# Performance work log

Hardware: AMD Instinct MI355X
Metric: run time of the kernel (lower is better)

The kernel has to match this reference:

```python
import jax, jax.numpy as jnp
import numpy as np

B_SIZE, STEPS, UNITS = 128, 1024, 1024
E = 2 * STEPS              # model_internal_dim = expand_factor * model_input_dims
DT_RANK = (STEPS + 1) // 2 # math.ceil(model_input_dims / 2)
N = UNITS // 2             # model_states
COND = 512                 # conditioning feature size
K = 4                      # conv kernel size


def setup_inputs() -> dict:
    key = jax.random.key(0)
    ks = jax.random.split(key, 12)
    s = lambda k, shape, fan: jax.random.normal(k, shape, jnp.float32) / np.sqrt(fan)
    return {
        "x": jax.random.normal(ks[0], (B_SIZE, 1, STEPS), jnp.float32),
        "c": jax.random.normal(ks[1], (B_SIZE, COND), jnp.float32),
        "ln_g": jnp.ones((STEPS,), jnp.float32),
        "ln_b": jnp.zeros((STEPS,), jnp.float32),
        "W_in": s(ks[2], (STEPS, 2 * E), STEPS),
        "conv_w": s(ks[3], (K, 1, E), K),
        "conv_b": jnp.zeros((E,), jnp.float32),
        "W_x": s(ks[4], (E, DT_RANK + 2 * N), E),
        "W_dt": s(ks[5], (DT_RANK, E), DT_RANK),
        "b_dt": jnp.zeros((E,), jnp.float32),
        "A_log": jnp.log(jnp.tile(jnp.arange(1, N + 1, dtype=jnp.float32), (E, 1))),
        "D": jnp.ones((E,), jnp.float32),
        "W_out": s(ks[6], (E, STEPS), E),
        "b_out": jnp.zeros((STEPS,), jnp.float32),
        "W_d": s(ks[7], (STEPS, N), STEPS),
        "b_d": jnp.zeros((N,), jnp.float32),
        "W_f": s(ks[8], (COND, 2 * N), COND),
        "b_f": jnp.zeros((2 * N,), jnp.float32),
        "W_o": s(ks[9], (N, STEPS), N),
        "b_o": jnp.zeros((STEPS,), jnp.float32),
    }


def _selective_scan(u, delta, A, Bm, Cm, D):
    # u, delta: (b,l,e); A: (e,n); Bm, Cm: (b,l,n); D: (e,)
    dA = jnp.exp(jnp.einsum('ble,en->blen', delta, A))        # discretized A
    dBu = jnp.einsum('ble,ble,bln->blen', delta, u, Bm)       # discretized B*u

    def step(h, t):
        dA_t, dBu_t, C_t = t
        h = dA_t * h + dBu_t                                  # (b,e,n)
        return h, jnp.einsum('ben,bn->be', h, C_t)

    h0 = jnp.zeros((dA.shape[0], dA.shape[2], dA.shape[3]), dA.dtype)
    _, ys = jax.lax.scan(step, h0, (dA.transpose(1, 0, 2, 3),
                                    dBu.transpose(1, 0, 2, 3),
                                    Cm.transpose(1, 0, 2)))
    y = ys.transpose(1, 0, 2)                                 # (b,l,e)
    return y + u * D


def reference(x, c, ln_g, ln_b, W_in, conv_w, conv_b, W_x, W_dt, b_dt,
              A_log, D, W_out, b_out, W_d, b_d, W_f, b_f, W_o, b_o):
    # --- ResidualBlock: LayerNorm -> MambaBlock -> + x ---
    mu = jnp.mean(x, -1, keepdims=True)
    var = jnp.var(x, -1, keepdims=True)
    h = (x - mu) * jax.lax.rsqrt(var + 1e-5) * ln_g + ln_b
    xz = h @ W_in                                             # (b,l,2E)
    xi, res = jnp.split(xz, 2, axis=-1)
    xc = jax.lax.conv_general_dilated(
        xi, conv_w, window_strides=(1,), padding=[(K - 1, 0)],
        dimension_numbers=('NWC', 'WIO', 'NWC'), feature_group_count=E) + conv_b
    u = jax.nn.silu(xc)
    x_dbl = u @ W_x                                           # (b,l,dt_rank+2N)
    d_r, Bm, Cm = jnp.split(x_dbl, [DT_RANK, DT_RANK + N], axis=-1)
    delta = jax.nn.softplus(d_r @ W_dt + b_dt)                # (b,l,E)
    A = -jnp.exp(A_log)
    y = _selective_scan(u, delta, A, Bm, Cm, D)
    y = y * jax.nn.silu(res)                                  # gating branch
    mamba_out = y @ W_out + b_out + x                         # residual add
    # --- Dense(model_states, gelu) then squeeze seq dim ---
    z = jax.nn.gelu(mamba_out @ W_d + b_d, approximate=False)
    z = jnp.squeeze(z, axis=1)                                # (b, N)
    # --- FiLM conditioning ---
    gb = c @ W_f + b_f
    g, b = jnp.split(gb, 2, axis=-1)
    z = z * g + b
    # --- output projection back to steps ---
    return z @ W_o + b_o
```

## Files before the change

kernel.cpp:

```cpp
#include <hip/hip_runtime.h>
#include <math.h>

#define E_DIM 2048

typedef __attribute__((ext_vector_type(8))) short short8;
typedef __attribute__((ext_vector_type(4))) float floatx4;

__device__ __forceinline__ float siluf(float v) { return v / (1.f + expf(-v)); }

__device__ __forceinline__ short f2bf(float f) {
    unsigned u = __float_as_uint(f);
    u += 0x7fffu + ((u >> 16) & 1u);
    return (short)(u >> 16);
}

__global__ __launch_bounds__(256) void ln_zero_kernel(const float* __restrict__ x,
                                                      const float* __restrict__ g,
                                                      const float* __restrict__ be,
                                                      const float* __restrict__ c,
                                                      short* __restrict__ h_bf,
                                                      short* __restrict__ c_bf,
                                                      float4* __restrict__ zbase,
                                                      int zTotal) {
    int tid = threadIdx.x;
    if (blockIdx.x < 128) {
        int b = blockIdx.x;
        __shared__ float sdata[256];
        const float* xr = x + b * 1024;
        float v[4];
        float s = 0.f;
#pragma unroll
        for (int i = 0; i < 4; ++i) { v[i] = xr[tid + i * 256]; s += v[i]; }
        sdata[tid] = s; __syncthreads();
        for (int st = 128; st > 0; st >>= 1) { if (tid < st) sdata[tid] += sdata[tid + st]; __syncthreads(); }
        float mu = sdata[0] * (1.f / 1024.f);
        __syncthreads();
        float s2 = 0.f;
#pragma unroll
        for (int i = 0; i < 4; ++i) { float d = v[i] - mu; s2 += d * d; }
        sdata[tid] = s2; __syncthreads();
        for (int st = 128; st > 0; st >>= 1) { if (tid < st) sdata[tid] += sdata[tid + st]; __syncthreads(); }
        float var = sdata[0] * (1.f / 1024.f);
        float inv = rsqrtf(var + 1e-5f);
        short* hr = h_bf + b * 1024;
#pragma unroll
        for (int i = 0; i < 4; ++i) {
            int j = tid + i * 256;
            hr[j] = f2bf((v[i] - mu) * inv * g[j] + be[j]);
        }
        const float* cr = c + b * 512;
        short* cbr = c_bf + b * 512;
        for (int j = tid; j < 512; j += 256) cbr[j] = f2bf(cr[j]);
    } else {
        int base = (blockIdx.x - 128) * 2048 + tid;
        int stride = (gridDim.x - 128) * 2048;
        for (int idx = base; idx < zTotal; idx += stride) {
#pragma unroll
            for (int i = 0; i < 8; ++i) {
                int k = idx + i * 256;
                if (k < zTotal) zbase[k] = (float4){0.f, 0.f, 0.f, 0.f};
            }
        }
    }
}

template<int MODE>
__device__ __forceinline__ short8 load_a_frag(const void* __restrict__ A, int lda, int r, int j0,
                                              const float* __restrict__ aux0,
                                              const float* __restrict__ aux1,
                                              const float* __restrict__ aux2) {
    if constexpr (MODE == 0) {
        return *(const short8*)((const short*)A + (size_t)r * lda + j0);
    } else {
        const float* p = (const float*)A + (size_t)r * lda + j0;
        float v[8];
        if constexpr (MODE == 1) {
#pragma unroll
            for (int i = 0; i < 8; ++i) v[i] = siluf(p[i] * aux0[j0 + i] + aux1[j0 + i]);
        } else if constexpr (MODE == 2) {
#pragma unroll
            for (int i = 0; i < 8; ++i) v[i] = p[i];
        } else if constexpr (MODE == 3) {
#pragma unroll
            for (int i = 0; i < 8; ++i) v[i] = p[i] + aux0[j0 + i] + aux1[(size_t)r * lda + j0 + i];
        } else {
#pragma unroll
            for (int i = 0; i < 8; ++i) {
                float t = p[i] + aux0[j0 + i];
                float zg = 0.5f * t * (1.f + erff(t * 0.70710678118654752f));
                float gq = aux1[(size_t)r * 1024 + j0 + i] + aux2[j0 + i];
                float bb = aux1[(size_t)r * 1024 + 512 + j0 + i] + aux2[512 + j0 + i];
                v[i] = zg * gq + bb;
            }
        }
        short8 s;
#pragma unroll
        for (int i = 0; i < 8; ++i) s[i] = f2bf(v[i]);
        return s;
    }
}

template<int MODE>
__global__ __launch_bounds__(256) void gemm_mfma(const void* __restrict__ A, int lda,
                                                 const float* __restrict__ aux0,
                                                 const float* __restrict__ aux1,
                                                 const float* __restrict__ aux2,
                                                 const float* __restrict__ B, int ldb,
                                                 float* __restrict__ C, int ldc,
                                                 int kChunk) {
    const int tid = threadIdx.x;
    const int w = tid >> 6;
    const int l = tid & 63;
    const int lane15 = l & 15;
    const int lgrp = l >> 4;
    const int n0 = blockIdx.x * 64;
    const int k0 = blockIdx.z * kChunk;

    const int r0 = w * 32 + lane15;
    const float* Bp = B + (size_t)(k0 + lgrp * 8) * ldb + n0 + lane15;

    floatx4 acc[2][4];
#pragma unroll
    for (int i = 0; i < 2; ++i)
#pragma unroll
        for (int j = 0; j < 4; ++j) acc[i][j] = (floatx4)0.f;

    for (int ks = 0; ks < kChunk; ks += 32) {
        int j0 = k0 + ks + lgrp * 8;
        short8 a0 = load_a_frag<MODE>(A, lda, r0, j0, aux0, aux1, aux2);
        short8 a1 = load_a_frag<MODE>(A, lda, r0 + 16, j0, aux0, aux1, aux2);
        float bv[4][8];
#pragma unroll
        for (int i = 0; i < 8; ++i) {
            const float* Br = Bp + i * ldb;
#pragma unroll
            for (int nt = 0; nt < 4; ++nt) bv[nt][i] = Br[nt * 16];
        }
        Bp += 32 * (size_t)ldb;
        short8 vb[4];
#pragma unroll
        for (int nt = 0; nt < 4; ++nt)
#pragma unroll
            for (int i = 0; i < 8; ++i) vb[nt][i] = f2bf(bv[nt][i]);
#pragma unroll
        for (int nt = 0; nt < 4; ++nt) {
            acc[0][nt] = __builtin_amdgcn_mfma_f32_16x16x32_bf16(a0, vb[nt], acc[0][nt], 0, 0, 0);
            acc[1][nt] = __builtin_amdgcn_mfma_f32_16x16x32_bf16(a1, vb[nt], acc[1][nt], 0, 0, 0);
        }
    }
    const int rbase = w * 32 + lgrp * 4;
#pragma unroll
    for (int mf = 0; mf < 2; ++mf)
#pragma unroll
        for (int nt = 0; nt < 4; ++nt)
#pragma unroll
            for (int r = 0; r < 4; ++r)
                atomicAdd(&C[(rbase + mf * 16 + r) * ldc + n0 + nt * 16 + lane15], acc[mf][nt][r]);
}

__global__ __launch_bounds__(256) void e3_kernel(const float* __restrict__ dacc,
                                                 const float* __restrict__ b_dt,
                                                 const float* __restrict__ xz,
                                                 const float* __restrict__ convw3,
                                                 const float* __restrict__ convb,
                                                 const float* __restrict__ xdbl,
                                                 const float* __restrict__ Dv,
                                                 short* __restrict__ y_bf) {
    int b = blockIdx.x;
    int tid = threadIdx.x;
    __shared__ float sdata[256];
    const float* row = xdbl + b * 1536;
    float s = 0.f;
    for (int n = tid; n < 512; n += 256) s += row[512 + n] * row[1024 + n];
    sdata[tid] = s; __syncthreads();
    for (int st = 128; st > 0; st >>= 1) { if (tid < st) sdata[tid] += sdata[tid + st]; __syncthreads(); }
    float svec = sdata[0];
    const float* xzr = xz + b * 4096;
    const float* dar = dacc + b * 2048;
    short* yr = y_bf + b * 2048;
#pragma unroll
    for (int ii = 0; ii < 8; ++ii) {
        int j = tid + ii * 256;
        float t = dar[j] + b_dt[j];
        float delta = fmaxf(t, 0.f) + log1pf(expf(-fabsf(t)));
        float u = siluf(xzr[j] * convw3[j] + convb[j]);
        float sr = siluf(xzr[2048 + j]);
        yr[j] = f2bf(u * (delta * svec + Dv[j]) * sr);
    }
}

__global__ __launch_bounds__(256) void e6_kernel(const float* __restrict__ oa,
                                                 const float* __restrict__ b_o,
                                                 float* __restrict__ out) {
    int idx = blockIdx.x * 256 + threadIdx.x;
    int j = idx & 1023;
    out[idx] = oa[idx] + b_o[j];
}

extern "C" void kernel_launch(void* const* d_in, const int* in_sizes, int n_in,
                              void* d_out, int out_size, void* d_ws, size_t ws_size,
                              hipStream_t stream) {
    (void)in_sizes; (void)n_in; (void)out_size; (void)ws_size;
    const float* x     = (const float*)d_in[0];
    const float* c     = (const float*)d_in[1];
    const float* ln_g  = (const float*)d_in[2];
    const float* ln_b  = (const float*)d_in[3];
    const float* W_in  = (const float*)d_in[4];
    const float* convw = (const float*)d_in[5];
    const float* convb = (const float*)d_in[6];
    const float* W_x   = (const float*)d_in[7];
    const float* W_dt  = (const float*)d_in[8];
    const float* b_dt  = (const float*)d_in[9];
    const float* Dv    = (const float*)d_in[11];
    const float* W_out = (const float*)d_in[12];
    const float* b_out = (const float*)d_in[13];
    const float* W_d   = (const float*)d_in[14];
    const float* b_d   = (const float*)d_in[15];
    const float* W_f   = (const float*)d_in[16];
    const float* b_f   = (const float*)d_in[17];
    const float* W_o   = (const float*)d_in[18];
    const float* b_o   = (const float*)d_in[19];
    float* out = (float*)d_out;

    char* ws = (char*)d_ws;
    size_t off = 0;
    auto allocf = [&](size_t nElem) { float* p = (float*)(ws + off); off += nElem * sizeof(float); return p; };
    auto allocs = [&](size_t nElem) { short* p = (short*)(ws + off); off += nElem * sizeof(short); return p; };
    float* xz_acc   = allocf(128 * 4096);
    float* xdbl_acc = allocf(128 * 1536);
    float* dacc     = allocf(128 * 2048);
    float* mo_acc   = allocf(128 * 1024);
    float* zd_acc   = allocf(128 * 512);
    float* gb_acc   = allocf(128 * 1024);
    float* out_acc  = allocf(128 * 1024);
    size_t accBytes = off;
    int zTotal = (int)(accBytes / 16);
    short* h_bf   = allocs(128 * 1024);
    short* c_bf   = allocs(128 * 512);
    short* y_bf   = allocs(128 * 2048);

    ln_zero_kernel<<<128 + 176, 256, 0, stream>>>(x, ln_g, ln_b, c, h_bf, c_bf,
                                                  (float4*)d_ws, zTotal);
    gemm_mfma<0><<<dim3(64, 1, 4), 256, 0, stream>>>(h_bf, 1024, nullptr, nullptr, nullptr,
                                                     W_in, 4096, xz_acc, 4096, 256);
    gemm_mfma<0><<<dim3(16, 1, 8), 256, 0, stream>>>(c_bf, 512, nullptr, nullptr, nullptr,
                                                     W_f, 1024, gb_acc, 1024, 64);
    gemm_mfma<1><<<dim3(24, 1, 8), 256, 0, stream>>>(xz_acc, 4096, convw + 3 * E_DIM, convb, nullptr,
                                                     W_x, 1536, xdbl_acc, 1536, 256);
    gemm_mfma<2><<<dim3(32, 1, 8), 256, 0, stream>>>(xdbl_acc, 1536, nullptr, nullptr, nullptr,
                                                     W_dt, 2048, dacc, 2048, 64);
    e3_kernel<<<128, 256, 0, stream>>>(dacc, b_dt, xz_acc, convw + 3 * E_DIM, convb,
                                       xdbl_acc, Dv, y_bf);
    gemm_mfma<0><<<dim3(16, 1, 8), 256, 0, stream>>>(y_bf, 2048, nullptr, nullptr, nullptr,
                                                     W_out, 1024, mo_acc, 1024, 256);
    gemm_mfma<3><<<dim3(8, 1, 16), 256, 0, stream>>>(mo_acc, 1024, b_out, x, nullptr,
                                                     W_d, 512, zd_acc, 512, 64);
    gemm_mfma<4><<<dim3(16, 1, 8), 256, 0, stream>>>(zd_acc, 512, b_d, gb_acc, b_f,
                                                     W_o, 1024, out_acc, 1024, 64);
    e6_kernel<<<(128 * 1024) / 256, 256, 0, stream>>>(out_acc, b_o, out);
}
```

Before: 103.9 us.

## Fuse pipeline into one persistent kernel with grid barriers and split-K partial buffers

Replaces the chain of ten kernel launches with a single persistent kernel of 256 blocks. Stages are separated by atomic-counter grid barriers. Split-K results are no longer accumulated with float atomics into zeroed buffers. Each K-slice writes a private partial buffer, and the consumer stage sums the slices, which removes the zeroing pass and atomic contention. The cost is extra partial-buffer memory traffic, barrier spin overhead, and reliance on all 256 blocks being co-resident.

```diff
diff --git a/kernel.cpp b/kernel.cpp
--- a/kernel.cpp
+++ b/kernel.cpp
@@ -1,10 +1,10 @@
 #include <hip/hip_runtime.h>
 #include <math.h>
 
-#define E_DIM 2048
-
 typedef __attribute__((ext_vector_type(8))) short short8;
 typedef __attribute__((ext_vector_type(4))) float floatx4;
+
+#define NBLK 256
 
 __device__ __forceinline__ float siluf(float v) { return v / (1.f + expf(-v)); }
 
@@ -14,18 +14,142 @@
     return (short)(u >> 16);
 }
 
-__global__ __launch_bounds__(256) void ln_zero_kernel(const float* __restrict__ x,
-                                                      const float* __restrict__ g,
-                                                      const float* __restrict__ be,
-                                                      const float* __restrict__ c,
-                                                      short* __restrict__ h_bf,
-                                                      short* __restrict__ c_bf,
-                                                      float4* __restrict__ zbase,
-                                                      int zTotal) {
-    int tid = threadIdx.x;
-    if (blockIdx.x < 128) {
-        int b = blockIdx.x;
-        __shared__ float sdata[256];
+__global__ void init_kernel(int* bar) {
+    if (threadIdx.x < 16) bar[threadIdx.x] = 0;
+}
+
+__device__ __forceinline__ void gbar(int* bar, int i) {
+    __syncthreads();
+    if (threadIdx.x == 0) {
+        __threadfence();
+        int old = __hip_atomic_fetch_add(&bar[i], 1, __ATOMIC_ACQ_REL, __HIP_MEMORY_SCOPE_AGENT);
+        if (old != NBLK - 1) {
+            while (__hip_atomic_load(&bar[i], __ATOMIC_RELAXED, __HIP_MEMORY_SCOPE_AGENT) < NBLK)
+                __builtin_amdgcn_s_sleep(1);
+        }
+        __threadfence();
+    }
+    __syncthreads();
+}
+
+template<int MODE, int NSUM>
+__device__ __forceinline__ short8 a_frag(const void* __restrict__ A, int lda, size_t ss,
+                                         int r, int j0,
+                                         const float* __restrict__ aux0,
+                                         const float* __restrict__ aux1) {
+    if constexpr (MODE == 0) {
+        return *(const short8*)((const short*)A + (size_t)r * lda + j0);
+    } else {
+        const float* Af = (const float*)A;
+        size_t base = (size_t)r * lda + j0;
+        float v[8];
+#pragma unroll
+        for (int i = 0; i < 8; ++i) {
+            float t;
+            if constexpr (MODE == 1) {
+                t = Af[base + i] + Af[ss + base + i];
+                t = siluf(t * aux0[j0 + i] + aux1[j0 + i]);
+            } else {
+                t = 0.f;
+#pragma unroll
+                for (int s = 0; s < NSUM; ++s) t += Af[(size_t)s * ss + base + i];
+                if constexpr (MODE == 3) t += aux0[j0 + i] + aux1[base + i];
+            }
+            v[i] = t;
+        }
+        short8 sv;
+#pragma unroll
+        for (int i = 0; i < 8; ++i) sv[i] = f2bf(v[i]);
+        return sv;
+    }
+}
+
+template<int MODE, int NSUM>
+__device__ __forceinline__ void gemm_stage(const void* __restrict__ A, int lda, size_t ss,
+                                           const float* __restrict__ aux0,
+                                           const float* __restrict__ aux1,
+                                           const float* __restrict__ B, int ldb,
+                                           float* __restrict__ Cs, int ldc,
+                                           int n0, int k0, int kSteps) {
+    const int tid = threadIdx.x;
+    const int w = tid >> 6;
+    const int l = tid & 63;
+    const int lane15 = l & 15;
+    const int lgrp = l >> 4;
+    const int r0 = w * 32 + lane15;
+    const float* Bp = B + (size_t)(k0 + lgrp * 8) * ldb + n0 + lane15;
+
+    floatx4 acc[2][4];
+#pragma unroll
+    for (int i = 0; i < 2; ++i)
+#pragma unroll
+        for (int j = 0; j < 4; ++j) acc[i][j] = (floatx4)0.f;
+
+    for (int s = 0; s < kSteps; ++s) {
+        int j0 = k0 + s * 32 + lgrp * 8;
+        short8 a0 = a_frag<MODE, NSUM>(A, lda, ss, r0, j0, aux0, aux1);
+        short8 a1 = a_frag<MODE, NSUM>(A, lda, ss, r0 + 16, j0, aux0, aux1);
+        float bv[4][8];
+#pragma unroll
+        for (int i = 0; i < 8; ++i) {
+            const float* Br = Bp + (size_t)i * ldb;
+#pragma unroll
+            for (int nt = 0; nt < 4; ++nt) bv[nt][i] = Br[nt * 16];
+        }
+        Bp += 32 * (size_t)ldb;
+        short8 vb[4];
+#pragma unroll
+        for (int nt = 0; nt < 4; ++nt)
+#pragma unroll
+            for (int i = 0; i < 8; ++i) vb[nt][i] = f2bf(bv[nt][i]);
+#pragma unroll
+        for (int nt = 0; nt < 4; ++nt) {
+            acc[0][nt] = __builtin_amdgcn_mfma_f32_16x16x32_bf16(a0, vb[nt], acc[0][nt], 0, 0, 0);
+            acc[1][nt] = __builtin_amdgcn_mfma_f32_16x16x32_bf16(a1, vb[nt], acc[1][nt], 0, 0, 0);
+        }
+    }
+    const int rbase = w * 32 + lgrp * 4;
+#pragma unroll
+    for (int mf = 0; mf < 2; ++mf)
+#pragma unroll
+        for (int nt = 0; nt < 4; ++nt)
+#pragma unroll
+            for (int r = 0; r < 4; ++r)
+                Cs[(size_t)(rbase + mf * 16 + r) * ldc + n0 + nt * 16 + lane15] = acc[mf][nt][r];
+}
+
+__global__ __launch_bounds__(256, 2) void uber_kernel(
+        const float* __restrict__ x, const float* __restrict__ c,
+        const float* __restrict__ ln_g, const float* __restrict__ ln_b,
+        const float* __restrict__ W_in, const float* __restrict__ cw3,
+        const float* __restrict__ cb, const float* __restrict__ W_x,
+        const float* __restrict__ W_dt, const float* __restrict__ b_dt,
+        const float* __restrict__ Dv, const float* __restrict__ W_out,
+        const float* __restrict__ b_out, const float* __restrict__ W_d,
+        const float* __restrict__ b_d, const float* __restrict__ W_f,
+        const float* __restrict__ b_f, const float* __restrict__ W_o,
+        const float* __restrict__ b_o, float* __restrict__ out,
+        int* __restrict__ bar,
+        short* __restrict__ h_bf, short* __restrict__ c_bf,
+        float* __restrict__ xz_p, float* __restrict__ gb_p,
+        float* __restrict__ xdbl_p, float* __restrict__ dacc_p,
+        short* __restrict__ y_bf, float* __restrict__ mo_p,
+        float* __restrict__ zd_p, short* __restrict__ z_bf,
+        float* __restrict__ out_p) {
+    const int bid = blockIdx.x;
+    const int tid = threadIdx.x;
+    __shared__ float sdata[256];
+
+    const size_t XZ_SL = (size_t)128 * 4096;
+    const size_t GB_SL = (size_t)128 * 1024;
+    const size_t XD_SL = (size_t)128 * 1536;
+    const size_t DA_SL = (size_t)128 * 2048;
+    const size_t MO_SL = (size_t)128 * 1024;
+    const size_t ZD_SL = (size_t)128 * 512;
+    const size_t OU_SL = (size_t)128 * 1024;
+
+    if (bid < 128) {
+        int b = bid;
         const float* xr = x + b * 1024;
         float v[4];
         float s = 0.f;
@@ -40,161 +164,129 @@
         for (int i = 0; i < 4; ++i) { float d = v[i] - mu; s2 += d * d; }
         sdata[tid] = s2; __syncthreads();
         for (int st = 128; st > 0; st >>= 1) { if (tid < st) sdata[tid] += sdata[tid + st]; __syncthreads(); }
-        float var = sdata[0] * (1.f / 1024.f);
-        float inv = rsqrtf(var + 1e-5f);
+        float inv = rsqrtf(sdata[0] * (1.f / 1024.f) + 1e-5f);
         short* hr = h_bf + b * 1024;
 #pragma unroll
         for (int i = 0; i < 4; ++i) {
             int j = tid + i * 256;
-            hr[j] = f2bf((v[i] - mu) * inv * g[j] + be[j]);
-        }
+            hr[j] = f2bf((v[i] - mu) * inv * ln_g[j] + ln_b[j]);
+        }
+    } else {
+        int b = bid - 128;
         const float* cr = c + b * 512;
         short* cbr = c_bf + b * 512;
-        for (int j = tid; j < 512; j += 256) cbr[j] = f2bf(cr[j]);
+        cbr[tid] = f2bf(cr[tid]);
+        cbr[tid + 256] = f2bf(cr[tid + 256]);
+    }
+    gbar(bar, 0);
+
+    if (bid < 128) {
+        int nb = bid >> 1, ks = bid & 1;
+        gemm_stage<0, 0>(h_bf, 1024, 0, nullptr, nullptr, W_in, 4096,
+                         xz_p + (size_t)ks * XZ_SL, 4096, nb * 64, ks * 512, 16);
     } else {
-        int base = (blockIdx.x - 128) * 2048 + tid;
-        int stride = (gridDim.x - 128) * 2048;
-        for (int idx = base; idx < zTotal; idx += stride) {
-#pragma unroll
-            for (int i = 0; i < 8; ++i) {
-                int k = idx + i * 256;
-                if (k < zTotal) zbase[k] = (float4){0.f, 0.f, 0.f, 0.f};
+        int t = bid - 128;
+        int nb = t >> 3, ks = t & 7;
+        gemm_stage<0, 0>(c_bf, 512, 0, nullptr, nullptr, W_f, 1024,
+                         gb_p + (size_t)ks * GB_SL, 1024, nb * 64, ks * 64, 2);
+    }
+    gbar(bar, 1);
+
+    if (bid < 192) {
+        int nb = bid >> 3, ks = bid & 7;
+        gemm_stage<1, 2>(xz_p, 4096, XZ_SL, cw3, cb, W_x, 1536,
+                         xdbl_p + (size_t)ks * XD_SL, 1536, nb * 64, ks * 256, 8);
+    }
+    gbar(bar, 2);
+
+    {
+        int nb = bid >> 3, ks = bid & 7;
+        gemm_stage<2, 8>(xdbl_p, 1536, XD_SL, nullptr, nullptr, W_dt, 2048,
+                         dacc_p + (size_t)ks * DA_SL, 2048, nb * 64, ks * 64, 2);
+    }
+    gbar(bar, 3);
+
+    {
+        int row = bid >> 1, half = bid & 1;
+        float s = 0.f;
+#pragma unroll
+        for (int q = 0; q < 2; ++q) {
+            int n = tid + q * 256;
+            float bm = 0.f, cm = 0.f;
+#pragma unroll
+            for (int sl = 0; sl < 8; ++sl) {
+                bm += xdbl_p[(size_t)sl * XD_SL + (size_t)row * 1536 + 512 + n];
+                cm += xdbl_p[(size_t)sl * XD_SL + (size_t)row * 1536 + 1024 + n];
             }
-        }
-    }
-}
-
-template<int MODE>
-__device__ __forceinline__ short8 load_a_frag(const void* __restrict__ A, int lda, int r, int j0,
-                                              const float* __restrict__ aux0,
-                                              const float* __restrict__ aux1,
-                                              const float* __restrict__ aux2) {
-    if constexpr (MODE == 0) {
-        return *(const short8*)((const short*)A + (size_t)r * lda + j0);
-    } else {
-        const float* p = (const float*)A + (size_t)r * lda + j0;
-        float v[8];
-        if constexpr (MODE == 1) {
-#pragma unroll
-            for (int i = 0; i < 8; ++i) v[i] = siluf(p[i] * aux0[j0 + i] + aux1[j0 + i]);
-        } else if constexpr (MODE == 2) {
-#pragma unroll
-            for (int i = 0; i < 8; ++i) v[i] = p[i];
-        } else if constexpr (MODE == 3) {
-#pragma unroll
-            for (int i = 0; i < 8; ++i) v[i] = p[i] + aux0[j0 + i] + aux1[(size_t)r * lda + j0 + i];
-        } else {
-#pragma unroll
-            for (int i = 0; i < 8; ++i) {
-                float t = p[i] + aux0[j0 + i];
-                float zg = 0.5f * t * (1.f + erff(t * 0.70710678118654752f));
-                float gq = aux1[(size_t)r * 1024 + j0 + i] + aux2[j0 + i];
-                float bb = aux1[(size_t)r * 1024 + 512 + j0 + i] + aux2[512 + j0 + i];
-                v[i] = zg * gq + bb;
-            }
-        }
-        short8 s;
-#pragma unroll
-        for (int i = 0; i < 8; ++i) s[i] = f2bf(v[i]);
-        return s;
-    }
-}
-
-template<int MODE>
-__global__ __launch_bounds__(256) void gemm_mfma(const void* __restrict__ A, int lda,
-                                                 const float* __restrict__ aux0,
-                                                 const float* __restrict__ aux1,
-                                                 const float* __restrict__ aux2,
-                                                 const float* __restrict__ B, int ldb,
-                                                 float* __restrict__ C, int ldc,
-                                                 int kChunk) {
-    const int tid = threadIdx.x;
-    const int w = tid >> 6;
-    const int l = tid & 63;
-    const int lane15 = l & 15;
-    const int lgrp = l >> 4;
-    const int n0 = blockIdx.x * 64;
-    const int k0 = blockIdx.z * kChunk;
-
-    const int r0 = w * 32 + lane15;
-    const float* Bp = B + (size_t)(k0 + lgrp * 8) * ldb + n0 + lane15;
-
-    floatx4 acc[2][4];
-#pragma unroll
-    for (int i = 0; i < 2; ++i)
-#pragma unroll
-        for (int j = 0; j < 4; ++j) acc[i][j] = (floatx4)0.f;
-
-    for (int ks = 0; ks < kChunk; ks += 32) {
-        int j0 = k0 + ks + lgrp * 8;
-        short8 a0 = load_a_frag<MODE>(A, lda, r0, j0, aux0, aux1, aux2);
-        short8 a1 = load_a_frag<MODE>(A, lda, r0 + 16, j0, aux0, aux1, aux2);
-        float bv[4][8];
-#pragma unroll
-        for (int i = 0; i < 8; ++i) {
-            const float* Br = Bp + i * ldb;
-#pragma unroll
-            for (int nt = 0; nt < 4; ++nt) bv[nt][i] = Br[nt * 16];
-        }
-        Bp += 32 * (size_t)ldb;
-        short8 vb[4];
-#pragma unroll
-        for (int nt = 0; nt < 4; ++nt)
-#pragma unroll
-            for (int i = 0; i < 8; ++i) vb[nt][i] = f2bf(bv[nt][i]);
-#pragma unroll
-        for (int nt = 0; nt < 4; ++nt) {
-            acc[0][nt] = __builtin_amdgcn_mfma_f32_16x16x32_bf16(a0, vb[nt], acc[0][nt], 0, 0, 0);
-            acc[1][nt] = __builtin_amdgcn_mfma_f32_16x16x32_bf16(a1, vb[nt], acc[1][nt], 0, 0, 0);
-        }
-    }
-    const int rbase = w * 32 + lgrp * 4;
-#pragma unroll
-    for (int mf = 0; mf < 2; ++mf)
-#pragma unroll
-        for (int nt = 0; nt < 4; ++nt)
-#pragma unroll
-            for (int r = 0; r < 4; ++r)
-                atomicAdd(&C[(rbase + mf * 16 + r) * ldc + n0 + nt * 16 + lane15], acc[mf][nt][r]);
-}
-
-__global__ __launch_bounds__(256) void e3_kernel(const float* __restrict__ dacc,
-                                                 const float* __restrict__ b_dt,
-                                                 const float* __restrict__ xz,
-                                                 const float* __restrict__ convw3,
-                                                 const float* __restrict__ convb,
-                                                 const float* __restrict__ xdbl,
-                                                 const float* __restrict__ Dv,
-                                                 short* __restrict__ y_bf) {
-    int b = blockIdx.x;
-    int tid = threadIdx.x;
-    __shared__ float sdata[256];
-    const float* row = xdbl + b * 1536;
-    float s = 0.f;
-    for (int n = tid; n < 512; n += 256) s += row[512 + n] * row[1024 + n];
-    sdata[tid] = s; __syncthreads();
-    for (int st = 128; st > 0; st >>= 1) { if (tid < st) sdata[tid] += sdata[tid + st]; __syncthreads(); }
-    float svec = sdata[0];
-    const float* xzr = xz + b * 4096;
-    const float* dar = dacc + b * 2048;
-    short* yr = y_bf + b * 2048;
-#pragma unroll
-    for (int ii = 0; ii < 8; ++ii) {
-        int j = tid + ii * 256;
-        float t = dar[j] + b_dt[j];
-        float delta = fmaxf(t, 0.f) + log1pf(expf(-fabsf(t)));
-        float u = siluf(xzr[j] * convw3[j] + convb[j]);
-        float sr = siluf(xzr[2048 + j]);
-        yr[j] = f2bf(u * (delta * svec + Dv[j]) * sr);
-    }
-}
-
-__global__ __launch_bounds__(256) void e6_kernel(const float* __restrict__ oa,
-                                                 const float* __restrict__ b_o,
-                                                 float* __restrict__ out) {
-    int idx = blockIdx.x * 256 + threadIdx.x;
-    int j = idx & 1023;
-    out[idx] = oa[idx] + b_o[j];
+            s += bm * cm;
+        }
+        sdata[tid] = s; __syncthreads();
+        for (int st = 128; st > 0; st >>= 1) { if (tid < st) sdata[tid] += sdata[tid + st]; __syncthreads(); }
+        float svec = sdata[0];
+        __syncthreads();
+#pragma unroll
+        for (int kk = 0; kk < 4; ++kk) {
+            int j = half * 1024 + tid + kk * 256;
+            float t = b_dt[j];
+#pragma unroll
+            for (int sl = 0; sl < 8; ++sl) t += dacc_p[(size_t)sl * DA_SL + (size_t)row * 2048 + j];
+            float delta = fmaxf(t, 0.f) + log1pf(expf(-fabsf(t)));
+            float xv = xz_p[(size_t)row * 4096 + j] + xz_p[XZ_SL + (size_t)row * 4096 + j];
+            float u = siluf(xv * cw3[j] + cb[j]);
+            float rv = xz_p[(size_t)row * 4096 + 2048 + j] + xz_p[XZ_SL + (size_t)row * 4096 + 2048 + j];
+            float sr = siluf(rv);
+            y_bf[(size_t)row * 2048 + j] = f2bf(u * (delta * svec + Dv[j]) * sr);
+        }
+    }
+    gbar(bar, 4);
+
+    if (bid < 128) {
+        int nb = bid >> 3, ks = bid & 7;
+        gemm_stage<0, 0>(y_bf, 2048, 0, nullptr, nullptr, W_out, 1024,
+                         mo_p + (size_t)ks * MO_SL, 1024, nb * 64, ks * 256, 8);
+    }
+    gbar(bar, 5);
+
+    if (bid < 128) {
+        int nb = bid >> 4, ks = bid & 15;
+        gemm_stage<3, 8>(mo_p, 1024, MO_SL, b_out, x, W_d, 512,
+                         zd_p + (size_t)ks * ZD_SL, 512, nb * 64, ks * 64, 2);
+    }
+    gbar(bar, 6);
+
+    {
+        int idx = bid * 256 + tid;
+        int row = idx >> 9, n = idx & 511;
+        float t = b_d[n];
+#pragma unroll
+        for (int sl = 0; sl < 16; ++sl) t += zd_p[(size_t)sl * ZD_SL + idx];
+        float zg = 0.5f * t * (1.f + erff(t * 0.70710678118654752f));
+        float gq = b_f[n], bb = b_f[512 + n];
+#pragma unroll
+        for (int sl = 0; sl < 8; ++sl) {
+            gq += gb_p[(size_t)sl * GB_SL + (size_t)row * 1024 + n];
+            bb += gb_p[(size_t)sl * GB_SL + (size_t)row * 1024 + 512 + n];
+        }
+        z_bf[idx] = f2bf(zg * gq + bb);
+    }
+    gbar(bar, 7);
+
+    {
+        int nb = bid >> 4, ks = bid & 15;
+        gemm_stage<0, 0>(z_bf, 512, 0, nullptr, nullptr, W_o, 1024,
+                         out_p + (size_t)ks * OU_SL, 1024, nb * 64, ks * 32, 1);
+    }
+    gbar(bar, 8);
+
+#pragma unroll
+    for (int q = 0; q < 2; ++q) {
+        int idx = bid * 512 + q * 256 + tid;
+        int j = idx & 1023;
+        float t = b_o[j];
+#pragma unroll
+        for (int sl = 0; sl < 16; ++sl) t += out_p[(size_t)sl * OU_SL + idx];
+        out[idx] = t;
+    }
 }
 
 extern "C" void kernel_launch(void* const* d_in, const int* in_sizes, int n_in,
@@ -224,38 +316,23 @@
 
     char* ws = (char*)d_ws;
     size_t off = 0;
-    auto allocf = [&](size_t nElem) { float* p = (float*)(ws + off); off += nElem * sizeof(float); return p; };
-    auto allocs = [&](size_t nElem) { short* p = (short*)(ws + off); off += nElem * sizeof(short); return p; };
-    float* xz_acc   = allocf(128 * 4096);
-    float* xdbl_acc = allocf(128 * 1536);
-    float* dacc     = allocf(128 * 2048);
-    float* mo_acc   = allocf(128 * 1024);
-    float* zd_acc   = allocf(128 * 512);
-    float* gb_acc   = allocf(128 * 1024);
-    float* out_acc  = allocf(128 * 1024);
-    size_t accBytes = off;
-    int zTotal = (int)(accBytes / 16);
-    short* h_bf   = allocs(128 * 1024);
-    short* c_bf   = allocs(128 * 512);
-    short* y_bf   = allocs(128 * 2048);
-
-    ln_zero_kernel<<<128 + 176, 256, 0, stream>>>(x, ln_g, ln_b, c, h_bf, c_bf,
-                                                  (float4*)d_ws, zTotal);
-    gemm_mfma<0><<<dim3(64, 1, 4), 256, 0, stream>>>(h_bf, 1024, nullptr, nullptr, nullptr,
-                                                     W_in, 4096, xz_acc, 4096, 256);
-    gemm_mfma<0><<<dim3(16, 1, 8), 256, 0, stream>>>(c_bf, 512, nullptr, nullptr, nullptr,
-                                                     W_f, 1024, gb_acc, 1024, 64);
-    gemm_mfma<1><<<dim3(24, 1, 8), 256, 0, stream>>>(xz_acc, 4096, convw + 3 * E_DIM, convb, nullptr,
-                                                     W_x, 1536, xdbl_acc, 1536, 256);
-    gemm_mfma<2><<<dim3(32, 1, 8), 256, 0, stream>>>(xdbl_acc, 1536, nullptr, nullptr, nullptr,
-                                                     W_dt, 2048, dacc, 2048, 64);
-    e3_kernel<<<128, 256, 0, stream>>>(dacc, b_dt, xz_acc, convw + 3 * E_DIM, convb,
-                                       xdbl_acc, Dv, y_bf);
-    gemm_mfma<0><<<dim3(16, 1, 8), 256, 0, stream>>>(y_bf, 2048, nullptr, nullptr, nullptr,
-                                                     W_out, 1024, mo_acc, 1024, 256);
-    gemm_mfma<3><<<dim3(8, 1, 16), 256, 0, stream>>>(mo_acc, 1024, b_out, x, nullptr,
-                                                     W_d, 512, zd_acc, 512, 64);
-    gemm_mfma<4><<<dim3(16, 1, 8), 256, 0, stream>>>(zd_acc, 512, b_d, gb_acc, b_f,
-                                                     W_o, 1024, out_acc, 1024, 64);
-    e6_kernel<<<(128 * 1024) / 256, 256, 0, stream>>>(out_acc, b_o, out);
-}
+    auto alloc = [&](size_t bytes) { void* p = ws + off; off += (bytes + 255) & ~(size_t)255; return p; };
+    int*   bar    = (int*)  alloc(16 * sizeof(int));
+    short* h_bf   = (short*)alloc(128 * 1024 * 2);
+    short* c_bf   = (short*)alloc(128 * 512 * 2);
+    float* xz_p   = (float*)alloc((size_t)2 * 128 * 4096 * 4);
+    float* gb_p   = (float*)alloc((size_t)8 * 128 * 1024 * 4);
+    float* xdbl_p = (float*)alloc((size_t)8 * 128 * 1536 * 4);
+    float* dacc_p = (float*)alloc((size_t)8 * 128 * 2048 * 4);
+    short* y_bf   = (short*)alloc(128 * 2048 * 2);
+    float* mo_p   = (float*)alloc((size_t)8 * 128 * 1024 * 4);
+    float* zd_p   = (float*)alloc((size_t)16 * 128 * 512 * 4);
+    short* z_bf   = (short*)alloc(128 * 512 * 2);
+    float* out_p  = (float*)alloc((size_t)16 * 128 * 1024 * 4);
+
+    init_kernel<<<1, 64, 0, stream>>>(bar);
+    uber_kernel<<<NBLK, 256, 0, stream>>>(
+        x, c, ln_g, ln_b, W_in, convw + 3 * 2048, convb, W_x, W_dt, b_dt,
+        Dv, W_out, b_out, W_d, b_d, W_f, b_f, W_o, b_o, out,
+        bar, h_bf, c_bf, xz_p, gb_p, xdbl_p, dacc_p, y_bf, mo_p, zd_p, z_bf, out_p);
+}
```

After: 310.6 us. 2.99x slower.
